# Kernel optimization log

Hardware: AMD Instinct MI355X
Metric: run time of the kernel (lower is better)

Reference implementation:

```python
import jax, jax.numpy as jnp
import numpy as np

N = 131072
MANO_CHILD = (2, 3, 17, 5, 6, 18, 8, 9, 20, 11, 12, 19, 14, 15, 16)
MANO_PARENT = (1, 2, 3, 4, 5, 6, 7, 8, 9, 10, 11, 12, 13, 14, 15)
FINGERS = ((0, 1, 2, 3, 17), (0, 4, 5, 6, 18), (0, 7, 8, 9, 20), (0, 10, 11, 12, 19), (0, 13, 14, 15, 16))
PALM = np.array([0, 1, 4, 7, 10, 13])
MAX_FLEX = float(np.pi / 2)  # flexion clamp range [0, pi/2]
EPS = 1e-8


def _wrist_rot(src, dst):
    """Kabsch rotation R (N,3,3) such that R @ src_k ~= dst_k (palm alignment)."""
    H = jnp.einsum('nki,nkj->nij', src, dst)          # sum_k src dst^T
    U, S, Vt = jnp.linalg.svd(H, full_matrices=False)
    VUt = jnp.einsum('nji,nkj->nik', Vt, U)           # V @ U^T
    d = jnp.linalg.det(VUt)
    D = jnp.stack([jnp.ones_like(d), jnp.ones_like(d), d], axis=-1)
    return jnp.einsum('nji,nj,nkj->nik', Vt, D, U)    # V diag(1,1,d) U^T


def _rodrigues(v, axis, theta):
    """Rotate vectors v (N,3) about unit axis (N,3) by angle theta (N,)."""
    c = jnp.cos(theta)[:, None]
    s = jnp.sin(theta)[:, None]
    return v * c + jnp.cross(axis, v) * s + axis * jnp.sum(axis * v, -1, keepdims=True) * (1.0 - c)


def _forward(joints, tempJ):
    wrist = joints[:, :1]
    J = joints - wrist                       # wrist-centered observed joints
    T = tempJ - tempJ[:, :1]                 # wrist-centered template
    bone_ref = T                             # bonelenTempJ: reference bone lengths
    # rigid palm alignment of template onto observed joints
    R = _wrist_rot(T[:, PALM], J[:, PALM])
    T = jnp.einsum('nij,nkj->nki', R, T)     # rotate every template joint
    # palm joints of observation are replaced by aligned template palm
    J = J.at[:, PALM].set(T[:, PALM])
    # (hand-pose-legitimize layer approximated as identity; source unavailable)
    for idx in range(len(MANO_CHILD)):
        ch, pa = MANO_CHILD[idx], MANO_PARENT[idx]
        v1 = J[:, ch] - T[:, pa]
        dis = jnp.linalg.norm(v1, axis=1)
        univ1 = v1 / (dis[:, None] + EPS)
        blen = jnp.linalg.norm(bone_ref[:, ch] - bone_ref[:, pa], axis=1)
        lo, hi = blen, blen                  # non-RHD template: lower == upper
        valid = (lo <= dis) & (dis <= hi)
        clamped = jnp.clip(dis, lo, hi)
        new = jnp.where(valid[:, None], J[:, ch], T[:, pa] + univ1 * clamped[:, None])
        T = T.at[:, ch].set(new)
        # flexion legitimization: clamp bend angle of this bone vs its parent bone
        f = FINGERS[idx // 3]
        k = idx % 3
        gp, pp, cc = f[k], f[k + 1], f[k + 2]  # grandparent, parent(=pa), child(=ch)
        v0 = T[:, pp] - T[:, gp]
        vb = T[:, cc] - T[:, pp]
        cr = jnp.cross(v0, vb)
        s = jnp.linalg.norm(cr, axis=1)
        c = jnp.sum(v0 * vb, axis=1)
        ang = jnp.arctan2(s, c)
        delta = jnp.clip(ang, 0.0, MAX_FLEX) - ang
        axis = cr / (s[:, None] + EPS)
        T = T.at[:, cc].set(_rodrigues(vb, axis, delta) + T[:, pp])
    return wrist + T


def setup_inputs() -> dict:
    key = jax.random.key(0)
    k1, k2 = jax.random.split(key)
    joints = jax.random.normal(k1, (N, 21, 3), dtype=jnp.float32)
    tempJ = jax.random.normal(k2, (N, 21, 3), dtype=jnp.float32)
    return {"joints": joints, "tempJ": tempJ}


def reference(joints, tempJ):
    return _forward(joints, tempJ)
```

## Files before the change

kernel.cpp:

```cpp
#include <hip/hip_runtime.h>
#include <math.h>

#define BLOCK 256
#define HF 63
#define TILE_F (BLOCK * HF)
#define TILE_V4 (TILE_F / 4)

__device__ __forceinline__ float rsqf(float x)  { return __builtin_amdgcn_rsqf(x); }
__device__ __forceinline__ float sqtf(float x)  { return __builtin_amdgcn_sqrtf(x); }

__global__ __launch_bounds__(BLOCK, 2)
void kin_fwd(const float* __restrict__ joints,
             const float* __restrict__ tempJ,
             float* __restrict__ out,
             int n_total)
{
    constexpr int CHILD[15]  = {2,3,17, 5,6,18, 8,9,20, 11,12,19, 14,15,16};
    constexpr int PARENT[15] = {1,2,3, 4,5,6, 7,8,9, 10,11,12, 13,14,15};
    constexpr int GPID[15]   = {0,1,2, 0,4,5, 0,7,8, 0,10,11, 0,13,14};
    constexpr int PALM[6]    = {0,1,4,7,10,13};

    __shared__ float lds[TILE_F];

    const int tid = threadIdx.x;
    const int n   = blockIdx.x * BLOCK + tid;
    const long long tileBase = (long long)blockIdx.x * TILE_F;
    const long long totalF   = (long long)n_total * HF;
    const bool fullTile = (tileBase + TILE_F) <= totalF;
    const bool active = (n < n_total);

    if (fullTile) {
        const float4* g4 = (const float4*)(tempJ + tileBase);
        float4* l4 = (float4*)lds;
        for (int idx = tid; idx < TILE_V4; idx += BLOCK) l4[idx] = g4[idx];
    } else {
        for (int idx = tid; idx < TILE_F; idx += BLOCK) {
            const long long g = tileBase + idx;
            lds[idx] = (g < totalF) ? tempJ[g] : 0.f;
        }
    }
    __syncthreads();

    float T[21][3];
    float blen[15];

    if (active) {
        const float* tl = lds + tid * HF;
#pragma unroll
        for (int k = 0; k < 21; ++k) {
            T[k][0] = tl[3*k+0];
            T[k][1] = tl[3*k+1];
            T[k][2] = tl[3*k+2];
        }
        const float ox = T[0][0], oy = T[0][1], oz = T[0][2];
#pragma unroll
        for (int k = 0; k < 21; ++k) { T[k][0] -= ox; T[k][1] -= oy; T[k][2] -= oz; }

#pragma unroll
        for (int i = 0; i < 15; ++i) {
            const float dx = T[CHILD[i]][0] - T[PARENT[i]][0];
            const float dy = T[CHILD[i]][1] - T[PARENT[i]][1];
            const float dz = T[CHILD[i]][2] - T[PARENT[i]][2];
            blen[i] = sqtf(dx*dx + dy*dy + dz*dz);
        }
    }
    __syncthreads();

    if (fullTile) {
        const float4* g4 = (const float4*)(joints + tileBase);
        float4* l4 = (float4*)lds;
        for (int idx = tid; idx < TILE_V4; idx += BLOCK) l4[idx] = g4[idx];
    } else {
        for (int idx = tid; idx < TILE_F; idx += BLOCK) {
            const long long g = tileBase + idx;
            lds[idx] = (g < totalF) ? joints[g] : 0.f;
        }
    }
    __syncthreads();

    float wx = 0.f, wy = 0.f, wz = 0.f;

    if (active) {
        float Jl[21][3];
        {
            const float* jl = lds + tid * HF;
            wx = jl[0]; wy = jl[1]; wz = jl[2];
#pragma unroll
            for (int k = 0; k < 21; ++k) {
                Jl[k][0] = jl[3*k+0] - wx;
                Jl[k][1] = jl[3*k+1] - wy;
                Jl[k][2] = jl[3*k+2] - wz;
            }
        }

        float H[3][3] = {{0.f,0.f,0.f},{0.f,0.f,0.f},{0.f,0.f,0.f}};
#pragma unroll
        for (int p = 0; p < 6; ++p) {
            const int k = PALM[p];
#pragma unroll
            for (int i = 0; i < 3; ++i)
#pragma unroll
                for (int j = 0; j < 3; ++j)
                    H[i][j] += T[k][i] * Jl[k][j];
        }

        float A[3][3];
#pragma unroll
        for (int i = 0; i < 3; ++i)
#pragma unroll
            for (int j = 0; j < 3; ++j)
                A[i][j] = H[0][i]*H[0][j] + H[1][i]*H[1][j] + H[2][i]*H[2][j];

        float V[3][3] = {{1.f,0.f,0.f},{0.f,1.f,0.f},{0.f,0.f,1.f}};
#pragma unroll
        for (int sw = 0; sw < 4; ++sw) {
#pragma unroll
            for (int r = 0; r < 3; ++r) {
                const int p = (r == 2) ? 1 : 0;
                const int q = (r == 0) ? 1 : 2;
                const float b   = A[p][q];
                const float dif = A[q][q] - A[p][p];
                const float irho = rsqf(dif*dif + 4.f*b*b + 1e-35f);
                const float c2  = dif * irho;
                const float c   = sqtf(fmaxf(0.5f + 0.5f*c2, 0.f));
                const float s   = copysignf(sqtf(fmaxf(0.5f - 0.5f*c2, 0.f)), b);
#pragma unroll
                for (int i = 0; i < 3; ++i) {
                    const float aip = A[i][p], aiq = A[i][q];
                    A[i][p] = c*aip - s*aiq;
                    A[i][q] = s*aip + c*aiq;
                }
#pragma unroll
                for (int j = 0; j < 3; ++j) {
                    const float apj = A[p][j], aqj = A[q][j];
                    A[p][j] = c*apj - s*aqj;
                    A[q][j] = s*apj + c*aqj;
                }
#pragma unroll
                for (int i = 0; i < 3; ++i) {
                    const float vip = V[i][p], viq = V[i][q];
                    V[i][p] = c*vip - s*viq;
                    V[i][q] = s*vip + c*viq;
                }
            }
        }

        float lam[3] = {A[0][0], A[1][1], A[2][2]};
#pragma unroll
        for (int pass = 0; pass < 3; ++pass) {
            const int i = (pass == 2) ? 1 : 0;
            const int j = (pass == 0) ? 1 : 2;
            if (lam[i] < lam[j]) {
                const float tl2 = lam[i]; lam[i] = lam[j]; lam[j] = tl2;
#pragma unroll
                for (int r2 = 0; r2 < 3; ++r2) {
                    const float tv = V[r2][i]; V[r2][i] = V[r2][j]; V[r2][j] = tv;
                }
            }
        }

        float R[3][3];
        {
            const float v1x = V[0][0], v1y = V[1][0], v1z = V[2][0];
            const float v2x = V[0][1], v2y = V[1][1], v2z = V[2][1];
            const float v3x = V[0][2], v3y = V[1][2], v3z = V[2][2];

            const float w1x = H[0][0]*v1x + H[0][1]*v1y + H[0][2]*v1z;
            const float w1y = H[1][0]*v1x + H[1][1]*v1y + H[1][2]*v1z;
            const float w1z = H[2][0]*v1x + H[2][1]*v1y + H[2][2]*v1z;
            const float in1 = rsqf(w1x*w1x + w1y*w1y + w1z*w1z + 1e-35f);
            const float u1x = w1x*in1, u1y = w1y*in1, u1z = w1z*in1;

            float w2x = H[0][0]*v2x + H[0][1]*v2y + H[0][2]*v2z;
            float w2y = H[1][0]*v2x + H[1][1]*v2y + H[1][2]*v2z;
            float w2z = H[2][0]*v2x + H[2][1]*v2y + H[2][2]*v2z;
            const float dp = u1x*w2x + u1y*w2y + u1z*w2z;
            w2x -= dp*u1x; w2y -= dp*u1y; w2z -= dp*u1z;
            const float in2 = rsqf(w2x*w2x + w2y*w2y + w2z*w2z + 1e-35f);
            const float u2x = w2x*in2, u2y = w2y*in2, u2z = w2z*in2;

            const float u3x = u1y*u2z - u1z*u2y;
            const float u3y = u1z*u2x - u1x*u2z;
            const float u3z = u1x*u2y - u1y*u2x;

            const float detV =
                v1x*(v2y*v3z - v2z*v3y) - v1y*(v2x*v3z - v2z*v3x) + v1z*(v2x*v3y - v2y*v3x);
            const float d = (detV < 0.f) ? -1.f : 1.f;
            const float w3x = d*v3x, w3y = d*v3y, w3z = d*v3z;

            R[0][0] = v1x*u1x + v2x*u2x + w3x*u3x;
            R[0][1] = v1x*u1y + v2x*u2y + w3x*u3y;
            R[0][2] = v1x*u1z + v2x*u2z + w3x*u3z;
            R[1][0] = v1y*u1x + v2y*u2x + w3y*u3x;
            R[1][1] = v1y*u1y + v2y*u2y + w3y*u3y;
            R[1][2] = v1y*u1z + v2y*u2z + w3y*u3z;
            R[2][0] = v1z*u1x + v2z*u2x + w3z*u3x;
            R[2][1] = v1z*u1y + v2z*u2y + w3z*u3y;
            R[2][2] = v1z*u1z + v2z*u2z + w3z*u3z;
        }

#pragma unroll
        for (int k = 0; k < 21; ++k) {
            const float x = T[k][0], y = T[k][1], z = T[k][2];
            T[k][0] = R[0][0]*x + R[0][1]*y + R[0][2]*z;
            T[k][1] = R[1][0]*x + R[1][1]*y + R[1][2]*z;
            T[k][2] = R[2][0]*x + R[2][1]*y + R[2][2]*z;
        }

#pragma unroll
        for (int i = 0; i < 15; ++i) {
            const int ch = CHILD[i], pa = PARENT[i], gp = GPID[i];

            const float v1x = Jl[ch][0] - T[pa][0];
            const float v1y = Jl[ch][1] - T[pa][1];
            const float v1z = Jl[ch][2] - T[pa][2];
            const float d2  = v1x*v1x + v1y*v1y + v1z*v1z;
            const float sc  = blen[i] * rsqf(d2 + 1e-16f);
            const float vbx = v1x*sc, vby = v1y*sc, vbz = v1z*sc;

            const float v0x = T[pa][0] - T[gp][0];
            const float v0y = T[pa][1] - T[gp][1];
            const float v0z = T[pa][2] - T[gp][2];

            const float crx = v0y*vbz - v0z*vby;
            const float cry = v0z*vbx - v0x*vbz;
            const float crz = v0x*vby - v0y*vbx;
            const float s2  = crx*crx + cry*cry + crz*crz;
            const float c   = v0x*vbx + v0y*vby + v0z*vbz;

            const float invr  = rsqf(s2 + c*c + 1e-35f);
            const float sainv = rsqf(s2 + 1e-35f);
            const float s     = s2 * sainv;
            const float cosd  = (c < 0.f) ? s*invr : 1.f;
            const float sind  = (c < 0.f) ? c*invr : 0.f;

            const float ax = crx*sainv, ay = cry*sainv, az = crz*sainv;
            const float cxx = ay*vbz - az*vby;
            const float cxy = az*vbx - ax*vbz;
            const float cxz = ax*vby - ay*vbx;
            T[ch][0] = vbx*cosd + cxx*sind + T[pa][0];
            T[ch][1] = vby*cosd + cxy*sind + T[pa][1];
            T[ch][2] = vbz*cosd + cxz*sind + T[pa][2];
        }

        float* ol = lds + tid * HF;
#pragma unroll
        for (int k = 0; k < 21; ++k) {
            ol[3*k+0] = wx + T[k][0];
            ol[3*k+1] = wy + T[k][1];
            ol[3*k+2] = wz + T[k][2];
        }
    }
    __syncthreads();

    if (fullTile) {
        float4* g4 = (float4*)(out + tileBase);
        const float4* l4 = (const float4*)lds;
        for (int idx = tid; idx < TILE_V4; idx += BLOCK) g4[idx] = l4[idx];
    } else {
        for (int idx = tid; idx < TILE_F; idx += BLOCK) {
            const long long g = tileBase + idx;
            if (g < totalF) out[g] = lds[idx];
        }
    }
}

extern "C" void kernel_launch(void* const* d_in, const int* in_sizes, int n_in,
                              void* d_out, int out_size, void* d_ws, size_t ws_size,
                              hipStream_t stream)
{
    const float* joints = (const float*)d_in[0];
    const float* tempJ  = (const float*)d_in[1];
    float* out          = (float*)d_out;

    const int n_total = in_sizes[0] / 63;
    const int grid = (n_total + BLOCK - 1) / BLOCK;
    kin_fwd<<<grid, BLOCK, 0, stream>>>(joints, tempJ, out, n_total);
}
```

Before: 111.3 us.

## Replace Jacobi eigen-solve with closed-form trigonometric eigendecomposition for Kabsch rotation

```diff
diff --git a/kernel.cpp b/kernel.cpp
--- a/kernel.cpp
+++ b/kernel.cpp
@@ -42,7 +42,7 @@
     __syncthreads();
 
     float T[21][3];
-    float blen[15];
+    float blen2[15];
 
     if (active) {
         const float* tl = lds + tid * HF;
@@ -61,7 +61,7 @@
             const float dx = T[CHILD[i]][0] - T[PARENT[i]][0];
             const float dy = T[CHILD[i]][1] - T[PARENT[i]][1];
             const float dz = T[CHILD[i]][2] - T[PARENT[i]][2];
-            blen[i] = sqtf(dx*dx + dy*dy + dz*dz);
+            blen2[i] = dx*dx + dy*dy + dz*dz;
         }
     }
     __syncthreads();
@@ -111,60 +111,104 @@
             for (int j = 0; j < 3; ++j)
                 A[i][j] = H[0][i]*H[0][j] + H[1][i]*H[1][j] + H[2][i]*H[2][j];
 
-        float V[3][3] = {{1.f,0.f,0.f},{0.f,1.f,0.f},{0.f,0.f,1.f}};
-#pragma unroll
-        for (int sw = 0; sw < 4; ++sw) {
-#pragma unroll
-            for (int r = 0; r < 3; ++r) {
-                const int p = (r == 2) ? 1 : 0;
-                const int q = (r == 0) ? 1 : 2;
-                const float b   = A[p][q];
-                const float dif = A[q][q] - A[p][p];
-                const float irho = rsqf(dif*dif + 4.f*b*b + 1e-35f);
-                const float c2  = dif * irho;
-                const float c   = sqtf(fmaxf(0.5f + 0.5f*c2, 0.f));
-                const float s   = copysignf(sqtf(fmaxf(0.5f - 0.5f*c2, 0.f)), b);
-#pragma unroll
-                for (int i = 0; i < 3; ++i) {
-                    const float aip = A[i][p], aiq = A[i][q];
-                    A[i][p] = c*aip - s*aiq;
-                    A[i][q] = s*aip + c*aiq;
-                }
-#pragma unroll
-                for (int j = 0; j < 3; ++j) {
-                    const float apj = A[p][j], aqj = A[q][j];
-                    A[p][j] = c*apj - s*aqj;
-                    A[q][j] = s*apj + c*aqj;
-                }
-#pragma unroll
-                for (int i = 0; i < 3; ++i) {
-                    const float vip = V[i][p], viq = V[i][q];
-                    V[i][p] = c*vip - s*viq;
-                    V[i][q] = s*vip + c*viq;
-                }
-            }
-        }
-
-        float lam[3] = {A[0][0], A[1][1], A[2][2]};
-#pragma unroll
-        for (int pass = 0; pass < 3; ++pass) {
-            const int i = (pass == 2) ? 1 : 0;
-            const int j = (pass == 0) ? 1 : 2;
-            if (lam[i] < lam[j]) {
-                const float tl2 = lam[i]; lam[i] = lam[j]; lam[j] = tl2;
-#pragma unroll
-                for (int r2 = 0; r2 < 3; ++r2) {
-                    const float tv = V[r2][i]; V[r2][i] = V[r2][j]; V[r2][j] = tv;
-                }
-            }
-        }
+        const float q   = (A[0][0] + A[1][1] + A[2][2]) * (1.f/3.f);
+        const float a00 = A[0][0]-q, a11 = A[1][1]-q, a22 = A[2][2]-q;
+        const float a01 = A[0][1], a02 = A[0][2], a12 = A[1][2];
+        const float p1  = a01*a01 + a02*a02 + a12*a12;
+        const float p2s = a00*a00 + a11*a11 + a22*a22 + 2.f*p1;
+        const float p26 = p2s*(1.f/6.f) + 1e-30f;
+        const float ip  = rsqf(p26);
+        const float p   = p26 * ip;
+        const float detC =
+            a00*(a11*a22 - a12*a12) - a01*(a01*a22 - a12*a02) + a02*(a01*a12 - a11*a02);
+        float r = 0.5f * detC * ip*ip*ip;
+        r = fminf(1.f, fmaxf(-1.f, r));
+        const float phi_rev = acosf(r) * 0.05305164769729845f;
+        const float cph = __builtin_amdgcn_cosf(phi_rev);
+        const float sph = __builtin_amdgcn_sinf(phi_rev);
+        const float e1 = q + 2.f*p*cph;
+        const float e3 = q - p*(cph + 1.7320508075688772f*sph);
+        const float e2 = 3.f*q - e1 - e3;
+
+        const float gap12 = e1 - e2, gap23 = e2 - e3;
+        const bool isoTop = (gap12 >= gap23);
+        const float sAB = isoTop ? (e2 + e3) : (e1 + e2);
+        const float pAB = isoTop ? (e2 * e3) : (e1 * e2);
+
+        const float A2_00 = A[0][0]*A[0][0] + A[0][1]*A[0][1] + A[0][2]*A[0][2];
+        const float A2_01 = A[0][0]*A[0][1] + A[0][1]*A[1][1] + A[0][2]*A[1][2];
+        const float A2_02 = A[0][0]*A[0][2] + A[0][1]*A[1][2] + A[0][2]*A[2][2];
+        const float A2_11 = A[0][1]*A[0][1] + A[1][1]*A[1][1] + A[1][2]*A[1][2];
+        const float A2_12 = A[0][1]*A[0][2] + A[1][1]*A[1][2] + A[1][2]*A[2][2];
+        const float A2_22 = A[0][2]*A[0][2] + A[1][2]*A[1][2] + A[2][2]*A[2][2];
+
+        const float m00 = A2_00 - sAB*A[0][0] + pAB;
+        const float m01 = A2_01 - sAB*A[0][1];
+        const float m02 = A2_02 - sAB*A[0][2];
+        const float m11 = A2_11 - sAB*A[1][1] + pAB;
+        const float m12 = A2_12 - sAB*A[1][2];
+        const float m22 = A2_22 - sAB*A[2][2] + pAB;
+
+        const float n0c = m00*m00 + m01*m01 + m02*m02;
+        const float n1c = m01*m01 + m11*m11 + m12*m12;
+        const float n2c = m02*m02 + m12*m12 + m22*m22;
+        float vx = m00, vy = m01, vz = m02, nb = n0c;
+        if (n1c > nb) { vx = m01; vy = m11; vz = m12; nb = n1c; }
+        if (n2c > nb) { vx = m02; vy = m12; vz = m22; nb = n2c; }
+        if (nb < 1e-24f) { vx = 1.f; vy = 0.f; vz = 0.f; }
+        {
+            const float invv = rsqf(vx*vx + vy*vy + vz*vz + 1e-35f);
+            vx *= invv; vy *= invv; vz *= invv;
+        }
+
+        float hx, hy, hz;
+        {
+            const float axv = fabsf(vx), ayv = fabsf(vy), azv = fabsf(vz);
+            if (axv <= ayv && axv <= azv)      { hx = 0.f;  hy = vz;  hz = -vy; }
+            else if (ayv <= azv)               { hx = -vz;  hy = 0.f; hz = vx;  }
+            else                               { hx = vy;   hy = -vx; hz = 0.f; }
+        }
+        const float invh = rsqf(hx*hx + hy*hy + hz*hz + 1e-35f);
+        const float b1x = hx*invh, b1y = hy*invh, b1z = hz*invh;
+        const float b2x = vy*b1z - vz*b1y;
+        const float b2y = vz*b1x - vx*b1z;
+        const float b2z = vx*b1y - vy*b1x;
+
+        const float Ab1x = A[0][0]*b1x + A[0][1]*b1y + A[0][2]*b1z;
+        const float Ab1y = A[0][1]*b1x + A[1][1]*b1y + A[1][2]*b1z;
+        const float Ab1z = A[0][2]*b1x + A[1][2]*b1y + A[2][2]*b1z;
+        const float Ab2x = A[0][0]*b2x + A[0][1]*b2y + A[0][2]*b2z;
+        const float Ab2y = A[0][1]*b2x + A[1][1]*b2y + A[1][2]*b2z;
+        const float Ab2z = A[0][2]*b2x + A[1][2]*b2y + A[2][2]*b2z;
+        const float alpha = b1x*Ab1x + b1y*Ab1y + b1z*Ab1z;
+        const float beta  = b2x*Ab1x + b2y*Ab1y + b2z*Ab1z;
+        const float gamma = b2x*Ab2x + b2y*Ab2y + b2z*Ab2z;
+
+        const float difq  = 0.5f*(alpha - gamma);
+        const float rootq = sqtf(difq*difq + beta*beta);
+        float tx = beta, ty = rootq - difq;
+        if (tx*tx + ty*ty < 1e-30f) { tx = 1.f; ty = 0.f; }
+        const float invt = rsqf(tx*tx + ty*ty + 1e-35f);
+        const float ctx = tx*invt, cty = ty*invt;
+        const float wpx = ctx*b1x + cty*b2x;
+        const float wpy = ctx*b1y + cty*b2y;
+        const float wpz = ctx*b1z + cty*b2z;
+        const float wmx = vy*wpz - vz*wpy;
+        const float wmy = vz*wpx - vx*wpz;
+        const float wmz = vx*wpy - vy*wpx;
+
+        const float v1x = isoTop ? vx  : wpx;
+        const float v1y = isoTop ? vy  : wpy;
+        const float v1z = isoTop ? vz  : wpz;
+        const float v2x = isoTop ? wpx : wmx;
+        const float v2y = isoTop ? wpy : wmy;
+        const float v2z = isoTop ? wpz : wmz;
+        const float v3x = v1y*v2z - v1z*v2y;
+        const float v3y = v1z*v2x - v1x*v2z;
+        const float v3z = v1x*v2y - v1y*v2x;
 
         float R[3][3];
         {
-            const float v1x = V[0][0], v1y = V[1][0], v1z = V[2][0];
-            const float v2x = V[0][1], v2y = V[1][1], v2z = V[2][1];
-            const float v3x = V[0][2], v3y = V[1][2], v3z = V[2][2];
-
             const float w1x = H[0][0]*v1x + H[0][1]*v1y + H[0][2]*v1z;
             const float w1y = H[1][0]*v1x + H[1][1]*v1y + H[1][2]*v1z;
             const float w1z = H[2][0]*v1x + H[2][1]*v1y + H[2][2]*v1z;
@@ -183,20 +227,15 @@
             const float u3y = u1z*u2x - u1x*u2z;
             const float u3z = u1x*u2y - u1y*u2x;
 
-            const float detV =
-                v1x*(v2y*v3z - v2z*v3y) - v1y*(v2x*v3z - v2z*v3x) + v1z*(v2x*v3y - v2y*v3x);
-            const float d = (detV < 0.f) ? -1.f : 1.f;
-            const float w3x = d*v3x, w3y = d*v3y, w3z = d*v3z;
-
-            R[0][0] = v1x*u1x + v2x*u2x + w3x*u3x;
-            R[0][1] = v1x*u1y + v2x*u2y + w3x*u3y;
-            R[0][2] = v1x*u1z + v2x*u2z + w3x*u3z;
-            R[1][0] = v1y*u1x + v2y*u2x + w3y*u3x;
-            R[1][1] = v1y*u1y + v2y*u2y + w3y*u3y;
-            R[1][2] = v1y*u1z + v2y*u2z + w3y*u3z;
-            R[2][0] = v1z*u1x + v2z*u2x + w3z*u3x;
-            R[2][1] = v1z*u1y + v2z*u2y + w3z*u3y;
-            R[2][2] = v1z*u1z + v2z*u2z + w3z*u3z;
+            R[0][0] = v1x*u1x + v2x*u2x + v3x*u3x;
+            R[0][1] = v1x*u1y + v2x*u2y + v3x*u3y;
+            R[0][2] = v1x*u1z + v2x*u2z + v3x*u3z;
+            R[1][0] = v1y*u1x + v2y*u2x + v3y*u3x;
+            R[1][1] = v1y*u1y + v2y*u2y + v3y*u3y;
+            R[1][2] = v1y*u1z + v2y*u2z + v3y*u3z;
+            R[2][0] = v1z*u1x + v2z*u2x + v3z*u3x;
+            R[2][1] = v1z*u1y + v2z*u2y + v3z*u3y;
+            R[2][2] = v1z*u1z + v2z*u2z + v3z*u3z;
         }
 
 #pragma unroll
@@ -211,12 +250,13 @@
         for (int i = 0; i < 15; ++i) {
             const int ch = CHILD[i], pa = PARENT[i], gp = GPID[i];
 
-            const float v1x = Jl[ch][0] - T[pa][0];
-            const float v1y = Jl[ch][1] - T[pa][1];
-            const float v1z = Jl[ch][2] - T[pa][2];
-            const float d2  = v1x*v1x + v1y*v1y + v1z*v1z;
-            const float sc  = blen[i] * rsqf(d2 + 1e-16f);
-            const float vbx = v1x*sc, vby = v1y*sc, vbz = v1z*sc;
+            const float v1xc = Jl[ch][0] - T[pa][0];
+            const float v1yc = Jl[ch][1] - T[pa][1];
+            const float v1zc = Jl[ch][2] - T[pa][2];
+            const float d2  = v1xc*v1xc + v1yc*v1yc + v1zc*v1zc;
+            const float b2  = blen2[i];
+            const float sc  = b2 * rsqf(b2*d2 + 1e-30f);
+            const float vbx = v1xc*sc, vby = v1yc*sc, vbz = v1zc*sc;
 
             const float v0x = T[pa][0] - T[gp][0];
             const float v0y = T[pa][1] - T[gp][1];
```

Result: no change. 110.5 us (-0.7%).
